# Kernel optimization log

Hardware: AMD Instinct MI355X
Metric: run time of the kernel (lower is better)

The kernel has to match this reference:

```python
import jax, jax.numpy as jnp
import numpy as np

V, E, H, B, S = 32000, 128, 256, 8, 512


def setup_inputs() -> dict:
    key = jax.random.key(0)
    ks = jax.random.split(key, 8)
    s_cell = 1.0 / np.sqrt(H)
    return {
        "t": jax.random.randint(ks[0], (B, S), 0, V),
        "emb": jax.random.normal(ks[1], (V, E), dtype=jnp.float32) * 0.02,
        "h0": jnp.zeros((1, H), dtype=jnp.float32),
        "w_ih": jax.random.uniform(ks[2], (3 * H, E), jnp.float32, -s_cell, s_cell),
        "w_hh": jax.random.uniform(ks[3], (3 * H, H), jnp.float32, -s_cell, s_cell),
        "b_ih": jax.random.uniform(ks[4], (3 * H,), jnp.float32, -s_cell, s_cell),
        "b_hh": jax.random.uniform(ks[5], (3 * H,), jnp.float32, -s_cell, s_cell),
        "w_out": jax.random.normal(ks[6], (V, H), dtype=jnp.float32) * 0.02,
        "b_out": jnp.zeros((V,), dtype=jnp.float32),
    }


def reference(t, emb, h0, w_ih, w_hh, b_ih, b_hh, w_out, b_out):
    x = emb[t]  # [B, S, E]
    # Input-side gate pre-activations can be batched over time (same math as per-step GRUCell)
    gi = jnp.einsum("bse,ge->bsg", x, w_ih) + b_ih  # [B, S, 3H]
    h_init = jnp.broadcast_to(h0, (t.shape[0], h0.shape[1]))  # [B, H]

    def step(h, gi_t):  # gi_t: [B, 3H]
        gh = h @ w_hh.T + b_hh  # [B, 3H]
        i_r, i_z, i_n = jnp.split(gi_t, 3, axis=-1)
        h_r, h_z, h_n = jnp.split(gh, 3, axis=-1)
        r = jax.nn.sigmoid(i_r + h_r)
        z = jax.nn.sigmoid(i_z + h_z)
        n = jnp.tanh(i_n + r * h_n)
        h_new = (1.0 - z) * n + z * h
        return h_new, h_new

    _, hs = jax.lax.scan(step, h_init, jnp.swapaxes(gi, 0, 1))  # hs: [S, B, H]
    hidden = jnp.swapaxes(hs, 0, 1)  # [B, S, H]
    return jnp.einsum("bsh,vh->bsv", hidden, w_out) + b_out  # [B, S, V]
```

## Files before the change

### kernel.cpp

```cpp
#include <hip/hip_runtime.h>
#include <stdint.h>


typedef __attribute__((ext_vector_type(8))) _Float16 half8;
typedef __attribute__((ext_vector_type(4))) _Float16 half4;
typedef __attribute__((ext_vector_type(4))) float float4v;
typedef __attribute__((ext_vector_type(4))) float facc4;
typedef __attribute__((ext_vector_type(4))) unsigned short ushort4v;

#define GI_BYTES   (512 * 8 * 768 * 4)
#define HID_BYTES  (4096 * 256 * 2)
#define FLAG_OFF   (GI_BYTES + HID_BYTES)

__device__ __forceinline__ float b2f(unsigned short u) {
  union { unsigned int i; float f; } v; v.i = ((unsigned int)u) << 16; return v.f;
}
__device__ __forceinline__ unsigned short f2b(float f) {
  union { float f; unsigned int i; } v; v.f = f;
  unsigned int r = v.i + 0x7FFFu + ((v.i >> 16) & 1u);
  return (unsigned short)(r >> 16);
}
template<bool BF> __device__ __forceinline__ float ldf(const void* p, int i) {
  if constexpr (BF) return b2f(((const unsigned short*)p)[i]);
  else              return ((const float*)p)[i];
}
template<bool BF> __device__ __forceinline__ float4v ld4(const void* p, int i) {
  float4v r;
  if constexpr (BF) {
    ushort4v u = *reinterpret_cast<const ushort4v*>((const unsigned short*)p + i);
#pragma unroll
    for (int j = 0; j < 4; ++j) r[j] = b2f(u[j]);
  } else {
    r = *reinterpret_cast<const float4v*>((const float*)p + i);
  }
  return r;
}

__global__ void k_detect(const unsigned int* __restrict__ emb_raw,
                         int* __restrict__ flag) {
  int tid = threadIdx.x;
  unsigned int u = emb_raw[tid];
  unsigned int lo = u & 0xFFFFu;
  unsigned int ex = (lo >> 7) & 0xFFu;
  int hit = ((ex >= 96u && ex <= 127u) || lo == 0u) ? 1 : 0;
  unsigned long long m = __ballot(hit);
  if (tid == 0) flag[0] = (__popcll(m) >= 40) ? 1 : 0;
}

template<bool BF>
__global__ __launch_bounds__(256, 4) void k_gi(
    const int* __restrict__ flag, const int* __restrict__ t,
    const void* __restrict__ emb, const void* __restrict__ w_ih,
    const void* __restrict__ b_ih, float* __restrict__ gi)
{
  if (*flag != (BF ? 1 : 0)) return;
  alignas(16) __shared__ float x_lds[4][128];
  const int n0 = blockIdx.x * 4;
  const int tid = threadIdx.x;
  for (int i = tid; i < 512; i += 256) {
    int tk = i >> 7, e = i & 127;
    int n = n0 + tk, s = n >> 3, b = n & 7;
    int tok = t[b * 512 + s];
    x_lds[tk][e] = ldf<BF>(emb, tok * 128 + e);
  }
  __syncthreads();
#pragma unroll
  for (int gg = 0; gg < 3; ++gg) {
    int g = gg * 256 + tid;
    float bias = ldf<BF>(b_ih, g);
    float a0 = bias, a1 = bias, a2 = bias, a3 = bias;
    for (int kb = 0; kb < 32; ++kb) {
      float4v w4 = ld4<BF>(w_ih, g * 128 + kb * 4);
#pragma unroll
      for (int j = 0; j < 4; ++j) {
        float w = w4[j]; int k = kb * 4 + j;
        a0 = fmaf(w, x_lds[0][k], a0);
        a1 = fmaf(w, x_lds[1][k], a1);
        a2 = fmaf(w, x_lds[2][k], a2);
        a3 = fmaf(w, x_lds[3][k], a3);
      }
    }
    gi[(n0 + 0) * 768 + g] = a0;
    gi[(n0 + 1) * 768 + g] = a1;
    gi[(n0 + 2) * 768 + g] = a2;
    gi[(n0 + 3) * 768 + g] = a3;
  }
}

template<bool BF>
__global__ __launch_bounds__(1024, 4) void k_scan(
    const int* __restrict__ flag, const void* __restrict__ w_hh,
    const void* __restrict__ b_hh, const void* __restrict__ h0,
    const float* __restrict__ gi, _Float16* __restrict__ hidden)
{
  if (*flag != (BF ? 1 : 0)) return;
  alignas(16) __shared__ _Float16 a_sh[2][256];
  alignas(16) __shared__ float gi_sh[2][768];
  alignas(16) __shared__ float bhh_sh[768];

  const int tid = threadIdx.x;
  const int b = blockIdx.x;
  const int wave = tid >> 6, lane = tid & 63;
  const int l15 = lane & 15, q = lane >> 4;
  const bool ard = (l15 == 0);
  const int qo = q * 8;

  half8 bfr[3][8];
#pragma unroll
  for (int tt = 0; tt < 3; ++tt) {
    int nrow = tt * 256 + (wave << 4) + l15;
#pragma unroll
    for (int kt = 0; kt < 8; ++kt) {
      int base = nrow * 256 + kt * 32 + qo;
      float4v x0 = ld4<BF>(w_hh, base), x1 = ld4<BF>(w_hh, base + 4);
      half8 h;
#pragma unroll
      for (int jj = 0; jj < 4; ++jj) { h[jj] = (_Float16)x0[jj]; h[4 + jj] = (_Float16)x1[jj]; }
      bfr[tt][kt] = h;
    }
  }

  if (tid < 768) bhh_sh[tid] = ldf<BF>(b_hh, tid);
  if (tid < 256) a_sh[0][tid] = (_Float16)ldf<BF>(h0, tid);
  if (tid < 768) gi_sh[0][tid] = gi[b * 768 + tid];
  float hreg = 0.f;
  if (lane < 16) hreg = ldf<BF>(h0, (wave << 4) + lane);

  half8 a0 = {}, a1 = {};
  _Float16* hid = hidden + b * 512 * 256;
  __syncthreads();

  int p = 0;
  for (int s = 0; s < 512; ++s) {
    float gnext = 0.f;
    if (tid < 768 && s < 511) gnext = gi[(s + 1) * 6144 + b * 768 + tid];

    const _Float16* ap = &a_sh[p][0];
    facc4 acc0 = {}, acc1 = {}, acc2 = {};
    if (ard) a0 = *reinterpret_cast<const half8*>(ap + qo);
#pragma unroll
    for (int kt = 0; kt < 8; kt += 2) {
      if (ard) a1 = *reinterpret_cast<const half8*>(ap + (kt + 1) * 32 + qo);
      acc0 = __builtin_amdgcn_mfma_f32_16x16x32_f16(a0, bfr[0][kt], acc0, 0, 0, 0);
      acc1 = __builtin_amdgcn_mfma_f32_16x16x32_f16(a0, bfr[1][kt], acc1, 0, 0, 0);
      acc2 = __builtin_amdgcn_mfma_f32_16x16x32_f16(a0, bfr[2][kt], acc2, 0, 0, 0);
      if (ard && kt + 2 < 8) a0 = *reinterpret_cast<const half8*>(ap + (kt + 2) * 32 + qo);
      acc0 = __builtin_amdgcn_mfma_f32_16x16x32_f16(a1, bfr[0][kt + 1], acc0, 0, 0, 0);
      acc1 = __builtin_amdgcn_mfma_f32_16x16x32_f16(a1, bfr[1][kt + 1], acc1, 0, 0, 0);
      acc2 = __builtin_amdgcn_mfma_f32_16x16x32_f16(a1, bfr[2][kt + 1], acc2, 0, 0, 0);
    }

    if (tid < 768 && s < 511) gi_sh[p ^ 1][tid] = gnext;

    if (lane < 16) {
      int j = (wave << 4) + lane;
      float ghr = acc0[0] + bhh_sh[j];
      float ghz = acc1[0] + bhh_sh[256 + j];
      float ghn = acc2[0] + bhh_sh[512 + j];
      float gir = gi_sh[p][j], giz = gi_sh[p][256 + j], gin = gi_sh[p][512 + j];
      float r = 1.f / (1.f + __expf(-(gir + ghr)));
      float z = 1.f / (1.f + __expf(-(giz + ghz)));
      float xn = gin + r * ghn;
      float e2 = __expf(2.f * xn);
      float nn = 1.f - 2.f / (e2 + 1.f);
      float hnew = (1.f - z) * nn + z * hreg;
      hreg = hnew;
      _Float16 hf = (_Float16)hnew;
      a_sh[p ^ 1][j] = hf;
      hid[s * 256 + j] = hf;
    }
    __syncthreads();
    p ^= 1;
  }
}

template<bool BF>
__global__ __launch_bounds__(256, 2) void k_out(
    const int* __restrict__ flag, const _Float16* __restrict__ hidden,
    const void* __restrict__ w_out, const void* __restrict__ b_out,
    void* __restrict__ out)
{
  if (*flag != (BF ? 1 : 0)) return;
  alignas(16) __shared__ _Float16 Asm[128 * 72];
  alignas(16) __shared__ _Float16 Bsm[128 * 72];
  const int bid = blockIdx.x;
  const int m0 = (bid & 31) * 128;
  const int n0 = (bid >> 5) * 128;
  const int tid = threadIdx.x;
  const int wave = tid >> 6, lane = tid & 63;
  const int l15 = lane & 15, q = lane >> 4;
  const int wm = (wave >> 1) * 64, wn = (wave & 1) * 64;

  facc4 acc[4][4] = {};
  float bo[4];
#pragma unroll
  for (int nt = 0; nt < 4; ++nt)
    bo[nt] = ldf<BF>(b_out, n0 + wn + nt * 16 + l15);

  for (int kk = 0; kk < 4; ++kk) {
    int k0 = kk * 64;
#pragma unroll
    for (int r = 0; r < 4; ++r) {
      int row = r * 32 + (tid >> 3);
      int ch = tid & 7;
      *reinterpret_cast<half8*>(&Asm[row * 72 + ch * 8]) =
          *reinterpret_cast<const half8*>(hidden + (m0 + row) * 256 + k0 + ch * 8);
      int wbase = (n0 + row) * 256 + k0 + ch * 8;
      float4v w0 = ld4<BF>(w_out, wbase), w1 = ld4<BF>(w_out, wbase + 4);
      half8 hB;
#pragma unroll
      for (int j = 0; j < 4; ++j) { hB[j] = (_Float16)w0[j]; hB[4 + j] = (_Float16)w1[j]; }
      *reinterpret_cast<half8*>(&Bsm[row * 72 + ch * 8]) = hB;
    }
    __syncthreads();
#pragma unroll
    for (int kt = 0; kt < 2; ++kt) {
      int koff = kt * 32 + q * 8;
      half8 af[4], bf[4];
#pragma unroll
      for (int mt = 0; mt < 4; ++mt)
        af[mt] = *reinterpret_cast<const half8*>(&Asm[(wm + mt * 16 + l15) * 72 + koff]);
#pragma unroll
      for (int nt = 0; nt < 4; ++nt)
        bf[nt] = *reinterpret_cast<const half8*>(&Bsm[(wn + nt * 16 + l15) * 72 + koff]);
#pragma unroll
      for (int mt = 0; mt < 4; ++mt)
#pragma unroll
        for (int nt = 0; nt < 4; ++nt)
          acc[mt][nt] = __builtin_amdgcn_mfma_f32_16x16x32_f16(
              af[mt], bf[nt], acc[mt][nt], 0, 0, 0);
    }
    __syncthreads();
  }
#pragma unroll
  for (int mt = 0; mt < 4; ++mt) {
#pragma unroll
    for (int i = 0; i < 4; ++i) {
      int row = m0 + wm + mt * 16 + q * 4 + i;
#pragma unroll
      for (int nt = 0; nt < 4; ++nt) {
        int col = n0 + wn + nt * 16 + l15;
        float val = acc[mt][nt][i] + bo[nt];
        if constexpr (BF) ((unsigned short*)out)[row * 32000 + col] = f2b(val);
        else              ((float*)out)[row * 32000 + col] = val;
      }
    }
  }
}

extern "C" void kernel_launch(void* const* d_in, const int* in_sizes, int n_in,
                              void* d_out, int out_size, void* d_ws, size_t ws_size,
                              hipStream_t stream) {
  const int* t     = (const int*)d_in[0];
  const void* emb  = d_in[1];
  const void* h0   = d_in[2];
  const void* w_ih = d_in[3];
  const void* w_hh = d_in[4];
  const void* b_ih = d_in[5];
  const void* b_hh = d_in[6];
  const void* w_out = d_in[7];
  const void* b_out = d_in[8];

  float*     gi     = (float*)d_ws;
  _Float16*  hidden = (_Float16*)((char*)d_ws + GI_BYTES);
  int*       flag   = (int*)((char*)d_ws + FLAG_OFF);

  k_detect<<<1, 64, 0, stream>>>((const unsigned int*)emb, flag);

  k_gi<false><<<1024, 256, 0, stream>>>(flag, t, emb, w_ih, b_ih, gi);
  k_gi<true> <<<1024, 256, 0, stream>>>(flag, t, emb, w_ih, b_ih, gi);

  k_scan<false><<<8, 1024, 0, stream>>>(flag, w_hh, b_hh, h0, gi, hidden);
  k_scan<true> <<<8, 1024, 0, stream>>>(flag, w_hh, b_hh, h0, gi, hidden);

  k_out<false><<<8000, 256, 0, stream>>>(flag, hidden, w_out, b_out, d_out);
  k_out<true> <<<8000, 256, 0, stream>>>(flag, hidden, w_out, b_out, d_out);
}
```

Before: 1.533 ms.

## Fold GRU hidden bias into MFMA accumulators, batch hidden stores, remap output blocks

The scan kernel keeps the hidden-side bias in registers and uses it as the initial MFMA accumulator value, which removes the shared-memory bias table and its per-step adds. The time loop is unrolled by 8 with the parity fixed at compile time, and each thread's hidden outputs are buffered and written to global memory once per 8 steps instead of every step. The output GEMM kernel permutes block indices so that 8 neighbouring launched blocks are spread across the grid, likely to suit XCD placement or L2 locality. The larger unroll and the hbuf array add register pressure in a kernel that already holds a large register-resident weight tile.

```diff
diff --git a/kernel.cpp b/kernel.cpp
--- a/kernel.cpp
+++ b/kernel.cpp
@@ -96,7 +96,6 @@
   if (*flag != (BF ? 1 : 0)) return;
   alignas(16) __shared__ _Float16 a_sh[2][256];
   alignas(16) __shared__ float gi_sh[2][768];
-  alignas(16) __shared__ float bhh_sh[768];
 
   const int tid = threadIdx.x;
   const int b = blockIdx.x;
@@ -104,11 +103,12 @@
   const int l15 = lane & 15, q = lane >> 4;
   const bool ard = (l15 == 0);
   const int qo = q * 8;
+  const int j = (wave << 4) + l15;
 
   half8 bfr[3][8];
 #pragma unroll
   for (int tt = 0; tt < 3; ++tt) {
-    int nrow = tt * 256 + (wave << 4) + l15;
+    int nrow = tt * 256 + j;
 #pragma unroll
     for (int kt = 0; kt < 8; ++kt) {
       int base = nrow * 256 + kt * 32 + qo;
@@ -120,57 +120,73 @@
     }
   }
 
-  if (tid < 768) bhh_sh[tid] = ldf<BF>(b_hh, tid);
+  const float bh_r = ldf<BF>(b_hh, j);
+  const float bh_z = ldf<BF>(b_hh, 256 + j);
+  const float bh_n = ldf<BF>(b_hh, 512 + j);
+
   if (tid < 256) a_sh[0][tid] = (_Float16)ldf<BF>(h0, tid);
   if (tid < 768) gi_sh[0][tid] = gi[b * 768 + tid];
-  float hreg = 0.f;
-  if (lane < 16) hreg = ldf<BF>(h0, (wave << 4) + lane);
+  float hreg = (lane < 16) ? ldf<BF>(h0, j) : 0.f;
 
   half8 a0 = {}, a1 = {};
+  _Float16 hbuf[8];
   _Float16* hid = hidden + b * 512 * 256;
   __syncthreads();
 
-  int p = 0;
-  for (int s = 0; s < 512; ++s) {
-    float gnext = 0.f;
-    if (tid < 768 && s < 511) gnext = gi[(s + 1) * 6144 + b * 768 + tid];
-
-    const _Float16* ap = &a_sh[p][0];
-    facc4 acc0 = {}, acc1 = {}, acc2 = {};
-    if (ard) a0 = *reinterpret_cast<const half8*>(ap + qo);
-#pragma unroll
-    for (int kt = 0; kt < 8; kt += 2) {
-      if (ard) a1 = *reinterpret_cast<const half8*>(ap + (kt + 1) * 32 + qo);
-      acc0 = __builtin_amdgcn_mfma_f32_16x16x32_f16(a0, bfr[0][kt], acc0, 0, 0, 0);
-      acc1 = __builtin_amdgcn_mfma_f32_16x16x32_f16(a0, bfr[1][kt], acc1, 0, 0, 0);
-      acc2 = __builtin_amdgcn_mfma_f32_16x16x32_f16(a0, bfr[2][kt], acc2, 0, 0, 0);
-      if (ard && kt + 2 < 8) a0 = *reinterpret_cast<const half8*>(ap + (kt + 2) * 32 + qo);
-      acc0 = __builtin_amdgcn_mfma_f32_16x16x32_f16(a1, bfr[0][kt + 1], acc0, 0, 0, 0);
-      acc1 = __builtin_amdgcn_mfma_f32_16x16x32_f16(a1, bfr[1][kt + 1], acc1, 0, 0, 0);
-      acc2 = __builtin_amdgcn_mfma_f32_16x16x32_f16(a1, bfr[2][kt + 1], acc2, 0, 0, 0);
-    }
-
-    if (tid < 768 && s < 511) gi_sh[p ^ 1][tid] = gnext;
-
-    if (lane < 16) {
-      int j = (wave << 4) + lane;
-      float ghr = acc0[0] + bhh_sh[j];
-      float ghz = acc1[0] + bhh_sh[256 + j];
-      float ghn = acc2[0] + bhh_sh[512 + j];
-      float gir = gi_sh[p][j], giz = gi_sh[p][256 + j], gin = gi_sh[p][512 + j];
-      float r = 1.f / (1.f + __expf(-(gir + ghr)));
-      float z = 1.f / (1.f + __expf(-(giz + ghz)));
-      float xn = gin + r * ghn;
-      float e2 = __expf(2.f * xn);
-      float nn = 1.f - 2.f / (e2 + 1.f);
-      float hnew = (1.f - z) * nn + z * hreg;
-      hreg = hnew;
-      _Float16 hf = (_Float16)hnew;
-      a_sh[p ^ 1][j] = hf;
-      hid[s * 256 + j] = hf;
-    }
-    __syncthreads();
-    p ^= 1;
+  for (int so = 0; so < 512; so += 8) {
+#pragma unroll
+    for (int u = 0; u < 8; ++u) {
+      const int s = so + u;
+      const int p = u & 1;
+
+      float gnext = 0.f;
+      if (tid < 768 && s < 511) gnext = gi[(s + 1) * 6144 + b * 768 + tid];
+
+      if (u == 0 && so > 0 && lane < 16) {
+#pragma unroll
+        for (int v = 0; v < 8; ++v)
+          hid[(so - 8 + v) * 256 + j] = hbuf[v];
+      }
+
+      const _Float16* ap = &a_sh[p][0];
+      facc4 acc0 = {bh_r, bh_r, bh_r, bh_r};
+      facc4 acc1 = {bh_z, bh_z, bh_z, bh_z};
+      facc4 acc2 = {bh_n, bh_n, bh_n, bh_n};
+      if (ard) a0 = *reinterpret_cast<const half8*>(ap + qo);
+#pragma unroll
+      for (int kt = 0; kt < 8; kt += 2) {
+        if (ard) a1 = *reinterpret_cast<const half8*>(ap + (kt + 1) * 32 + qo);
+        acc0 = __builtin_amdgcn_mfma_f32_16x16x32_f16(a0, bfr[0][kt], acc0, 0, 0, 0);
+        acc1 = __builtin_amdgcn_mfma_f32_16x16x32_f16(a0, bfr[1][kt], acc1, 0, 0, 0);
+        acc2 = __builtin_amdgcn_mfma_f32_16x16x32_f16(a0, bfr[2][kt], acc2, 0, 0, 0);
+        if (ard && kt + 2 < 8) a0 = *reinterpret_cast<const half8*>(ap + (kt + 2) * 32 + qo);
+        acc0 = __builtin_amdgcn_mfma_f32_16x16x32_f16(a1, bfr[0][kt + 1], acc0, 0, 0, 0);
+        acc1 = __builtin_amdgcn_mfma_f32_16x16x32_f16(a1, bfr[1][kt + 1], acc1, 0, 0, 0);
+        acc2 = __builtin_amdgcn_mfma_f32_16x16x32_f16(a1, bfr[2][kt + 1], acc2, 0, 0, 0);
+      }
+
+      if (tid < 768 && s < 511) gi_sh[p ^ 1][tid] = gnext;
+
+      if (lane < 16) {
+        float gir = gi_sh[p][j], giz = gi_sh[p][256 + j], gin = gi_sh[p][512 + j];
+        float r = 1.f / (1.f + __expf(-(gir + acc0[0])));
+        float z = 1.f / (1.f + __expf(-(giz + acc1[0])));
+        float xn = gin + r * acc2[0];
+        float e2 = __expf(2.f * xn);
+        float nn = 1.f - 2.f / (e2 + 1.f);
+        float hnew = (1.f - z) * nn + z * hreg;
+        hreg = hnew;
+        _Float16 hf = (_Float16)hnew;
+        a_sh[p ^ 1][j] = hf;
+        hbuf[u] = hf;
+      }
+      __syncthreads();
+    }
+  }
+  if (lane < 16) {
+#pragma unroll
+    for (int v = 0; v < 8; ++v)
+      hid[(504 + v) * 256 + j] = hbuf[v];
   }
 }
 
@@ -183,7 +199,8 @@
   if (*flag != (BF ? 1 : 0)) return;
   alignas(16) __shared__ _Float16 Asm[128 * 72];
   alignas(16) __shared__ _Float16 Bsm[128 * 72];
-  const int bid = blockIdx.x;
+  const int bid0 = blockIdx.x;
+  const int bid = (bid0 & 7) * 1000 + (bid0 >> 3);
   const int m0 = (bid & 31) * 128;
   const int n0 = (bid >> 5) * 128;
   const int tid = threadIdx.x;
@@ -209,7 +226,7 @@
       float4v w0 = ld4<BF>(w_out, wbase), w1 = ld4<BF>(w_out, wbase + 4);
       half8 hB;
 #pragma unroll
-      for (int j = 0; j < 4; ++j) { hB[j] = (_Float16)w0[j]; hB[4 + j] = (_Float16)w1[j]; }
+      for (int jj = 0; jj < 4; ++jj) { hB[jj] = (_Float16)w0[jj]; hB[4 + jj] = (_Float16)w1[jj]; }
       *reinterpret_cast<half8*>(&Bsm[row * 72 + ch * 8]) = hB;
     }
     __syncthreads();
```

After: 2.098 ms. +36.9%, slower.
